# Optimization experiments

Hardware: AMD Instinct MI355X
Metric: run time of the kernel (lower is better)

The kernel has to match this reference:

```python
import jax, jax.numpy as jnp
import numpy as np

B, S, D, H = 2, 4096, 512, 8
DH = D // H  # head dim = 64

def setup_inputs() -> dict:
    key = jax.random.key(0)
    ks = jax.random.split(key, 9)
    s = 0.02
    return {
        "Q": jax.random.normal(ks[0], (B, S, D), jnp.float32),
        "Wq": jax.random.normal(ks[1], (D, D), jnp.float32) * s,
        "bq": jnp.zeros((D,), jnp.float32),
        "Wk": jax.random.normal(ks[2], (D, D), jnp.float32) * s,
        "bk": jnp.zeros((D,), jnp.float32),
        "Wv": jax.random.normal(ks[3], (D, D), jnp.float32) * s,
        "bv": jnp.zeros((D,), jnp.float32),
        "Wo": jax.random.normal(ks[4], (D, D), jnp.float32) * s,
        "bo": jnp.zeros((D,), jnp.float32),
    }

def reference(Q, Wq, bq, Wk, bk, Wv, bv, Wo, bo):
    bs, s, d = Q.shape
    scale = DH ** -0.5
    # torch Linear: x @ W.T + b, W is [out, in]
    q = (Q @ Wq.T + bq).reshape(bs, s, H, DH).transpose(0, 2, 1, 3)  # [b,h,s,dh]
    k = (Q @ Wk.T + bk).reshape(bs, s, H, DH).transpose(0, 2, 1, 3)
    v = (Q @ Wv.T + bv).reshape(bs, s, H, DH).transpose(0, 2, 1, 3)
    scores = jnp.einsum('bhqd,bhkd->bhqk', q, k) * scale  # [b,h,s,s]
    attn = jax.nn.softmax(scores, axis=-1)
    out = jnp.einsum('bhqk,bhkd->bhqd', attn, v)  # [b,h,s,dh]
    out = out.transpose(0, 2, 1, 3).reshape(bs, s, H * DH)
    out = out @ Wo.T + bo
    return (out, attn)
```

## Files before the change

### kernel.cpp

```cpp
#include <hip/hip_runtime.h>
#include <hip/hip_bf16.h>

#define B_  2
#define S_  4096
#define D_  512
#define H_  8
#define DH_ 64
#define BH_ 16
#define M_  (B_*S_)

typedef __attribute__((ext_vector_type(4))) float f32x4;
typedef __attribute__((ext_vector_type(8))) short s16x8;
typedef __attribute__((ext_vector_type(4))) short s16x4;

#define MFMA(A,Bv,C) __builtin_amdgcn_mfma_f32_16x16x32_bf16(A,Bv,C,0,0,0)

typedef const void __attribute__((address_space(1)))* gas_t;
typedef void __attribute__((address_space(3)))* las_t;
#define GLDS(gp, lp) __builtin_amdgcn_global_load_lds((gas_t)(gp), (las_t)(lp), 16, 0, 0)

static __device__ __forceinline__ unsigned short f2bf(float f){
    union { float f; unsigned int u; } v; v.f = f;
    unsigned int r = (v.u + 0x7FFFu + ((v.u >> 16) & 1u)) >> 16;
    return (unsigned short)r;
}
static __device__ __forceinline__ float bf2f(unsigned short b){
    union { unsigned int u; float f; } v; v.u = ((unsigned int)b) << 16;
    return v.f;
}

__global__ __launch_bounds__(256) void cvt_bf16(const float* __restrict__ src,
                                                unsigned short* __restrict__ dst, int n4){
    int i = blockIdx.x * 256 + threadIdx.x;
    if (i < n4){
        float4 v = reinterpret_cast<const float4*>(src)[i];
        ushort4 o;
        o.x = f2bf(v.x); o.y = f2bf(v.y); o.z = f2bf(v.z); o.w = f2bf(v.w);
        reinterpret_cast<ushort4*>(dst)[i] = o;
    }
}

__global__ __launch_bounds__(256) void gemm_bt(const unsigned short* __restrict__ A,
                                               const unsigned short* __restrict__ W,
                                               const float* __restrict__ bias,
                                               unsigned short* __restrict__ dst_bf,
                                               float* __restrict__ dst_f32){
    const int mt = blockIdx.x, nt0 = blockIdx.y;
    const int wave = threadIdx.x >> 6, lane = threadIdx.x & 63;
    const int g = lane >> 4, r16 = lane & 15;
    const unsigned short* Ap = A + (size_t)(mt*64 + wave*16 + r16) * 512;

    f32x4 acc[4];
    #pragma unroll
    for (int i = 0; i < 4; ++i) acc[i] = (f32x4){0.f,0.f,0.f,0.f};

    #pragma unroll
    for (int k0 = 0; k0 < 512; k0 += 64){
        s16x8 a0 = *(const s16x8*)(Ap + k0 + g*8);
        s16x8 a1 = *(const s16x8*)(Ap + k0 + 32 + g*8);
        #pragma unroll
        for (int nt = 0; nt < 4; ++nt){
            const unsigned short* Wp = W + (size_t)(nt0*64 + nt*16 + r16)*512 + k0 + g*8;
            s16x8 b0 = *(const s16x8*)(Wp);
            s16x8 b1 = *(const s16x8*)(Wp + 32);
            acc[nt] = MFMA(a0, b0, acc[nt]);
            acc[nt] = MFMA(a1, b1, acc[nt]);
        }
    }

    #pragma unroll
    for (int nt = 0; nt < 4; ++nt){
        const int col = nt0*64 + nt*16 + r16;
        const float bv = bias[col];
        #pragma unroll
        for (int r = 0; r < 4; ++r){
            const int orow = mt*64 + wave*16 + g*4 + r;
            float val = acc[nt][r] + bv;
            if (dst_f32){
                dst_f32[(size_t)orow*512 + col] = val;
            } else {
                const int b = orow >> 12, s = orow & 4095;
                const int h = col >> 6,  dh = col & 63;
                dst_bf[((size_t)(b*H_ + h)*S_ + s)*DH_ + dh] = f2bf(val);
            }
        }
    }
}

__global__ __launch_bounds__(256) void transpose_v(const unsigned short* __restrict__ vh,
                                                   unsigned short* __restrict__ vT){
    __shared__ unsigned short tile[64][65];
    const int bh = blockIdx.y, s0 = blockIdx.x * 64;
    const int t = threadIdx.x, c = t & 63, r4 = t >> 6;
    const unsigned short* src = vh + (size_t)bh*S_*DH_;
    #pragma unroll
    for (int i = 0; i < 16; ++i){
        int sr = i*4 + r4;
        tile[sr][c] = src[(size_t)(s0 + sr)*DH_ + c];
    }
    __syncthreads();
    unsigned short* dst = vT + (size_t)bh*DH_*S_;
    #pragma unroll
    for (int i = 0; i < 16; ++i){
        int d = i*4 + r4;
        dst[(size_t)d*S_ + s0 + c] = tile[c][d];
    }
}

__global__ __launch_bounds__(512, 4) void attn_fused(const unsigned short* __restrict__ qh,
                                                     const unsigned short* __restrict__ kh,
                                                     const unsigned short* __restrict__ vT,
                                                     float* __restrict__ attn,
                                                     unsigned short* __restrict__ ctx){
    __shared__ unsigned short Kb[2][64][64];
    __shared__ unsigned short Vb[2][64][64];
    __shared__ unsigned short Pbf[8][16][68];

    const int lin = blockIdx.y * 32 + blockIdx.x;
    const int nl  = (lin & 7) * 64 + (lin >> 3);
    const int qt  = nl & 31;
    const int bh  = nl >> 5;

    const int wave = threadIdx.x >> 6, lane = threadIdx.x & 63;
    const int g = lane >> 4, r16 = lane & 15;
    const float SCALE = 0.125f;

    const unsigned short* qbase = qh + (size_t)bh*S_*DH_;
    const unsigned short* kbase = kh + (size_t)bh*S_*DH_;
    const unsigned short* vbase = vT + (size_t)bh*DH_*S_;

    const int tr = wave*8 + (lane >> 3);
    const int cc = (lane & 7) ^ (tr & 7);
    unsigned short* kl[2] = { &Kb[0][wave*8][0], &Kb[1][wave*8][0] };
    unsigned short* vl[2] = { &Vb[0][wave*8][0], &Vb[1][wave*8][0] };

    const int sw = r16 & 7;
    const int c0 = (g ^ sw) * 8;
    const int c1 = ((4 + g) ^ sw) * 8;

    const int qrow = qt*128 + wave*16 + r16;
    s16x8 qa0 = *(const s16x8*)(qbase + (size_t)qrow*DH_ + g*8);
    s16x8 qa1 = *(const s16x8*)(qbase + (size_t)qrow*DH_ + 32 + g*8);

    GLDS(kbase + (size_t)tr*DH_ + cc*8, kl[0]);
    asm volatile("s_waitcnt vmcnt(0)" ::: "memory");
    __builtin_amdgcn_s_barrier();
    __builtin_amdgcn_sched_barrier(0);

    float lsum[4] = {0.f,0.f,0.f,0.f};
    for (int t = 0; t < 64; ++t){
        const int nxt = (t + 1) & 63;
        GLDS(kbase + (size_t)(nxt*64 + tr)*DH_ + cc*8, kl[(t&1)^1]);
        __builtin_amdgcn_sched_barrier(0);
        const unsigned short (*Kt)[64] = Kb[t&1];
        #pragma unroll
        for (int nt = 0; nt < 4; ++nt){
            const int row = nt*16 + r16;
            s16x8 b0 = *(const s16x8*)(&Kt[row][c0]);
            s16x8 b1 = *(const s16x8*)(&Kt[row][c1]);
            f32x4 acc = (f32x4){0.f,0.f,0.f,0.f};
            acc = MFMA(qa0, b0, acc);
            acc = MFMA(qa1, b1, acc);
            #pragma unroll
            for (int r = 0; r < 4; ++r) lsum[r] += __expf(acc[r]*SCALE);
        }
        asm volatile("s_waitcnt vmcnt(0)" ::: "memory");
        __builtin_amdgcn_s_barrier();
        __builtin_amdgcn_sched_barrier(0);
    }

    #pragma unroll
    for (int m = 1; m < 16; m <<= 1){
        #pragma unroll
        for (int r = 0; r < 4; ++r) lsum[r] += __shfl_xor(lsum[r], m, 64);
    }
    float inv[4];
    #pragma unroll
    for (int r = 0; r < 4; ++r) inv[r] = 1.0f / lsum[r];

    f32x4 oacc[4];
    #pragma unroll
    for (int i = 0; i < 4; ++i) oacc[i] = (f32x4){0.f,0.f,0.f,0.f};

    GLDS(vbase + (size_t)tr*S_ + cc*8, vl[0]);
    asm volatile("s_waitcnt vmcnt(0)" ::: "memory");
    __builtin_amdgcn_s_barrier();
    __builtin_amdgcn_sched_barrier(0);

    float* attnW = attn + ((size_t)bh*S_ + qt*128 + wave*16)*S_;
    unsigned short (*Pw)[68] = Pbf[wave];

    for (int t = 0; t < 64; ++t){
        const int nxt = (t + 1) & 63;
        GLDS(kbase + (size_t)(nxt*64 + tr)*DH_ + cc*8, kl[(t&1)^1]);
        GLDS(vbase + (size_t)tr*S_ + nxt*64 + cc*8,    vl[(t&1)^1]);
        __builtin_amdgcn_sched_barrier(0);
        const unsigned short (*Kt)[64] = Kb[t&1];
        const unsigned short (*Vt)[64] = Vb[t&1];

        f32x4 pacc[4];
        #pragma unroll
        for (int nt = 0; nt < 4; ++nt){
            const int row = nt*16 + r16;
            s16x8 b0 = *(const s16x8*)(&Kt[row][c0]);
            s16x8 b1 = *(const s16x8*)(&Kt[row][c1]);
            f32x4 acc = (f32x4){0.f,0.f,0.f,0.f};
            acc = MFMA(qa0, b0, acc);
            acc = MFMA(qa1, b1, acc);
            pacc[nt] = acc;
        }
        #pragma unroll
        for (int nt = 0; nt < 4; ++nt){
            #pragma unroll
            for (int r = 0; r < 4; ++r){
                float p = __expf(pacc[nt][r]*SCALE) * inv[r];
                Pw[g*4 + r][nt*16 + r16] = f2bf(p);
            }
        }
        s16x4 plo0 = *(const s16x4*)(&Pw[r16][g*8]);
        s16x4 phi0 = *(const s16x4*)(&Pw[r16][g*8 + 4]);
        s16x4 plo1 = *(const s16x4*)(&Pw[r16][32 + g*8]);
        s16x4 phi1 = *(const s16x4*)(&Pw[r16][32 + g*8 + 4]);
        s16x8 pa0 = __builtin_shufflevector(plo0, phi0, 0,1,2,3,4,5,6,7);
        s16x8 pa1 = __builtin_shufflevector(plo1, phi1, 0,1,2,3,4,5,6,7);
        #pragma unroll
        for (int i = 0; i < 4; ++i){
            const int row = i*4 + g;
            s16x4 pb = *(const s16x4*)(&Pw[row][r16*4]);
            f32x4 o;
            #pragma unroll
            for (int j = 0; j < 4; ++j) o[j] = bf2f((unsigned short)pb[j]);
            __builtin_nontemporal_store(o, (f32x4*)(attnW + (size_t)row*S_ + t*64 + r16*4));
        }
        #pragma unroll
        for (int nt = 0; nt < 4; ++nt){
            const int row = nt*16 + r16;
            s16x8 v0 = *(const s16x8*)(&Vt[row][c0]);
            s16x8 v1 = *(const s16x8*)(&Vt[row][c1]);
            oacc[nt] = MFMA(pa0, v0, oacc[nt]);
            oacc[nt] = MFMA(pa1, v1, oacc[nt]);
        }
        asm volatile("s_waitcnt vmcnt(4)" ::: "memory");
        __builtin_amdgcn_s_barrier();
        __builtin_amdgcn_sched_barrier(0);
    }

    const int b = bh >> 3, h = bh & 7;
    #pragma unroll
    for (int nt = 0; nt < 4; ++nt){
        #pragma unroll
        for (int r = 0; r < 4; ++r){
            const int qr = qt*128 + wave*16 + g*4 + r;
            ctx[(size_t)(b*S_ + qr)*D_ + h*64 + nt*16 + r16] = f2bf(oacc[nt][r]);
        }
    }
}

extern "C" void kernel_launch(void* const* d_in, const int* in_sizes, int n_in,
                              void* d_out, int out_size, void* d_ws, size_t ws_size,
                              hipStream_t stream){
    const float* Q  = (const float*)d_in[0];
    const float* Wq = (const float*)d_in[1];
    const float* bq = (const float*)d_in[2];
    const float* Wk = (const float*)d_in[3];
    const float* bk = (const float*)d_in[4];
    const float* Wv = (const float*)d_in[5];
    const float* bv = (const float*)d_in[6];
    const float* Wo = (const float*)d_in[7];
    const float* bo = (const float*)d_in[8];

    float* out  = (float*)d_out;
    float* attn = out + (size_t)M_*D_;

    unsigned short* Qbf = (unsigned short*)attn;
    unsigned short* Wqb = Qbf + (size_t)M_*D_;
    unsigned short* Wkb = Wqb + 512*512;
    unsigned short* Wvb = Wkb + 512*512;
    unsigned short* vh  = Wvb + 512*512;

    unsigned short* qhb = (unsigned short*)d_ws;
    unsigned short* khb = qhb + (size_t)BH_*S_*DH_;
    unsigned short* vTb = khb + (size_t)BH_*S_*DH_;
    unsigned short* ctx = vTb + (size_t)BH_*S_*DH_;
    unsigned short* Wob = ctx + (size_t)M_*D_;

    cvt_bf16<<<dim3(M_*D_/4/256), 256, 0, stream>>>(Q,  Qbf, M_*D_/4);
    cvt_bf16<<<dim3(512*512/4/256), 256, 0, stream>>>(Wq, Wqb, 512*512/4);
    cvt_bf16<<<dim3(512*512/4/256), 256, 0, stream>>>(Wk, Wkb, 512*512/4);
    cvt_bf16<<<dim3(512*512/4/256), 256, 0, stream>>>(Wv, Wvb, 512*512/4);
    cvt_bf16<<<dim3(512*512/4/256), 256, 0, stream>>>(Wo, Wob, 512*512/4);

    dim3 pg(M_/64, D_/64);
    gemm_bt<<<pg, 256, 0, stream>>>(Qbf, Wqb, bq, qhb, nullptr);
    gemm_bt<<<pg, 256, 0, stream>>>(Qbf, Wkb, bk, khb, nullptr);
    gemm_bt<<<pg, 256, 0, stream>>>(Qbf, Wvb, bv, vh,  nullptr);

    transpose_v<<<dim3(S_/64, BH_), 256, 0, stream>>>(vh, vTb);

    attn_fused<<<dim3(32, BH_), 512, 0, stream>>>(qhb, khb, vTb, attn, ctx);

    gemm_bt<<<pg, 256, 0, stream>>>(ctx, Wob, bo, nullptr, out);
}
```

Baseline: 421.3 us.

## Batch attention-probability stores across tile pairs, use exp2, merge weight conversions

The second attention pass now double-buffers the per-wave probability tile in LDS and writes the fp32 attention matrix every two tiles, so each row write covers 128 contiguous columns (512 bytes) and the stores overlap the next tile's compute. The P fragments for the PV MFMA are read with single 16-byte LDS loads instead of split loads. Exponentials use the hardware exp2 with the scale folded into a log2e constant, and the four weight conversions are merged into one launch. The vmcnt wait counts were adjusted to match, which risks ordering mistakes and uses more LDS.

```diff
diff --git a/kernel.cpp b/kernel.cpp
--- a/kernel.cpp
+++ b/kernel.cpp
@@ -18,6 +18,8 @@
 typedef const void __attribute__((address_space(1)))* gas_t;
 typedef void __attribute__((address_space(3)))* las_t;
 #define GLDS(gp, lp) __builtin_amdgcn_global_load_lds((gas_t)(gp), (las_t)(lp), 16, 0, 0)
+
+#define EXP_C 0.18033688011112042f
 
 static __device__ __forceinline__ unsigned short f2bf(float f){
     union { float f; unsigned int u; } v; v.f = f;
@@ -38,6 +40,24 @@
         o.x = f2bf(v.x); o.y = f2bf(v.y); o.z = f2bf(v.z); o.w = f2bf(v.w);
         reinterpret_cast<ushort4*>(dst)[i] = o;
     }
+}
+
+__global__ __launch_bounds__(256) void cvt_w4(const float* __restrict__ s0, const float* __restrict__ s1,
+                                              const float* __restrict__ s2, const float* __restrict__ s3,
+                                              unsigned short* __restrict__ d0, unsigned short* __restrict__ d1,
+                                              unsigned short* __restrict__ d2, unsigned short* __restrict__ d3){
+    const float* s; unsigned short* d;
+    switch (blockIdx.y){
+        case 0: s = s0; d = d0; break;
+        case 1: s = s1; d = d1; break;
+        case 2: s = s2; d = d2; break;
+        default: s = s3; d = d3; break;
+    }
+    int i = blockIdx.x * 256 + threadIdx.x;
+    float4 v = reinterpret_cast<const float4*>(s)[i];
+    ushort4 o;
+    o.x = f2bf(v.x); o.y = f2bf(v.y); o.z = f2bf(v.z); o.w = f2bf(v.w);
+    reinterpret_cast<ushort4*>(d)[i] = o;
 }
 
 __global__ __launch_bounds__(256) void gemm_bt(const unsigned short* __restrict__ A,
@@ -114,7 +134,7 @@
                                                      unsigned short* __restrict__ ctx){
     __shared__ unsigned short Kb[2][64][64];
     __shared__ unsigned short Vb[2][64][64];
-    __shared__ unsigned short Pbf[8][16][68];
+    __shared__ __align__(16) unsigned short Pbf[8][16][136];
 
     const int lin = blockIdx.y * 32 + blockIdx.x;
     const int nl  = (lin & 7) * 64 + (lin >> 3);
@@ -123,7 +143,6 @@
 
     const int wave = threadIdx.x >> 6, lane = threadIdx.x & 63;
     const int g = lane >> 4, r16 = lane & 15;
-    const float SCALE = 0.125f;
 
     const unsigned short* qbase = qh + (size_t)bh*S_*DH_;
     const unsigned short* kbase = kh + (size_t)bh*S_*DH_;
@@ -162,7 +181,8 @@
             acc = MFMA(qa0, b0, acc);
             acc = MFMA(qa1, b1, acc);
             #pragma unroll
-            for (int r = 0; r < 4; ++r) lsum[r] += __expf(acc[r]*SCALE);
+            for (int r = 0; r < 4; ++r)
+                lsum[r] += __builtin_amdgcn_exp2f(acc[r]*EXP_C);
         }
         asm volatile("s_waitcnt vmcnt(0)" ::: "memory");
         __builtin_amdgcn_s_barrier();
@@ -188,16 +208,13 @@
     __builtin_amdgcn_sched_barrier(0);
 
     float* attnW = attn + ((size_t)bh*S_ + qt*128 + wave*16)*S_;
-    unsigned short (*Pw)[68] = Pbf[wave];
-
-    for (int t = 0; t < 64; ++t){
-        const int nxt = (t + 1) & 63;
-        GLDS(kbase + (size_t)(nxt*64 + tr)*DH_ + cc*8, kl[(t&1)^1]);
-        GLDS(vbase + (size_t)tr*S_ + nxt*64 + cc*8,    vl[(t&1)^1]);
-        __builtin_amdgcn_sched_barrier(0);
+    unsigned short (*Pw)[136] = Pbf[wave];
+    const int sl = lane & 31, sh = lane >> 5;
+
+    auto compute_tile = [&](int t){
         const unsigned short (*Kt)[64] = Kb[t&1];
         const unsigned short (*Vt)[64] = Vb[t&1];
-
+        const int cb = (t&1)*64;
         f32x4 pacc[4];
         #pragma unroll
         for (int nt = 0; nt < 4; ++nt){
@@ -213,25 +230,12 @@
         for (int nt = 0; nt < 4; ++nt){
             #pragma unroll
             for (int r = 0; r < 4; ++r){
-                float p = __expf(pacc[nt][r]*SCALE) * inv[r];
-                Pw[g*4 + r][nt*16 + r16] = f2bf(p);
+                float p = __builtin_amdgcn_exp2f(pacc[nt][r]*EXP_C) * inv[r];
+                Pw[g*4 + r][cb + nt*16 + r16] = f2bf(p);
             }
         }
-        s16x4 plo0 = *(const s16x4*)(&Pw[r16][g*8]);
-        s16x4 phi0 = *(const s16x4*)(&Pw[r16][g*8 + 4]);
-        s16x4 plo1 = *(const s16x4*)(&Pw[r16][32 + g*8]);
-        s16x4 phi1 = *(const s16x4*)(&Pw[r16][32 + g*8 + 4]);
-        s16x8 pa0 = __builtin_shufflevector(plo0, phi0, 0,1,2,3,4,5,6,7);
-        s16x8 pa1 = __builtin_shufflevector(plo1, phi1, 0,1,2,3,4,5,6,7);
-        #pragma unroll
-        for (int i = 0; i < 4; ++i){
-            const int row = i*4 + g;
-            s16x4 pb = *(const s16x4*)(&Pw[row][r16*4]);
-            f32x4 o;
-            #pragma unroll
-            for (int j = 0; j < 4; ++j) o[j] = bf2f((unsigned short)pb[j]);
-            __builtin_nontemporal_store(o, (f32x4*)(attnW + (size_t)row*S_ + t*64 + r16*4));
-        }
+        s16x8 pa0 = *(const s16x8*)(&Pw[r16][cb + g*8]);
+        s16x8 pa1 = *(const s16x8*)(&Pw[r16][cb + 32 + g*8]);
         #pragma unroll
         for (int nt = 0; nt < 4; ++nt){
             const int row = nt*16 + r16;
@@ -240,10 +244,48 @@
             oacc[nt] = MFMA(pa0, v0, oacc[nt]);
             oacc[nt] = MFMA(pa1, v1, oacc[nt]);
         }
-        asm volatile("s_waitcnt vmcnt(4)" ::: "memory");
+    };
+
+    auto store_pair = [&](int tfirst){
+        #pragma unroll
+        for (int i = 0; i < 8; ++i){
+            const int row = i*2 + sh;
+            s16x4 pb = *(const s16x4*)(&Pw[row][sl*4]);
+            f32x4 o;
+            #pragma unroll
+            for (int j = 0; j < 4; ++j) o[j] = bf2f((unsigned short)pb[j]);
+            __builtin_nontemporal_store(o,
+                (f32x4*)(attnW + (size_t)row*S_ + tfirst*64 + sl*4));
+        }
+    };
+
+    GLDS(kbase + (size_t)(1*64 + tr)*DH_ + cc*8, kl[1]);
+    GLDS(vbase + (size_t)tr*S_ + 1*64 + cc*8,    vl[1]);
+    __builtin_amdgcn_sched_barrier(0);
+    compute_tile(0);
+    asm volatile("s_waitcnt vmcnt(0)" ::: "memory");
+    __builtin_amdgcn_s_barrier();
+    __builtin_amdgcn_sched_barrier(0);
+
+    for (int t = 1; t < 64; ++t){
+        const int nxt = (t + 1) & 63;
+        GLDS(kbase + (size_t)(nxt*64 + tr)*DH_ + cc*8, kl[(t&1)^1]);
+        GLDS(vbase + (size_t)tr*S_ + nxt*64 + cc*8,    vl[(t&1)^1]);
+        __builtin_amdgcn_sched_barrier(0);
+        if ((t & 1) == 0){
+            store_pair(t - 2);
+            __builtin_amdgcn_sched_barrier(0);
+        }
+        compute_tile(t);
+        if (t & 1){
+            asm volatile("s_waitcnt vmcnt(0)" ::: "memory");
+        } else {
+            asm volatile("s_waitcnt vmcnt(8)" ::: "memory");
+        }
         __builtin_amdgcn_s_barrier();
         __builtin_amdgcn_sched_barrier(0);
     }
+    store_pair(62);
 
     const int b = bh >> 3, h = bh & 7;
     #pragma unroll
@@ -284,11 +326,8 @@
     unsigned short* ctx = vTb + (size_t)BH_*S_*DH_;
     unsigned short* Wob = ctx + (size_t)M_*D_;
 
-    cvt_bf16<<<dim3(M_*D_/4/256), 256, 0, stream>>>(Q,  Qbf, M_*D_/4);
-    cvt_bf16<<<dim3(512*512/4/256), 256, 0, stream>>>(Wq, Wqb, 512*512/4);
-    cvt_bf16<<<dim3(512*512/4/256), 256, 0, stream>>>(Wk, Wkb, 512*512/4);
-    cvt_bf16<<<dim3(512*512/4/256), 256, 0, stream>>>(Wv, Wvb, 512*512/4);
-    cvt_bf16<<<dim3(512*512/4/256), 256, 0, stream>>>(Wo, Wob, 512*512/4);
+    cvt_bf16<<<dim3(M_*D_/4/256), 256, 0, stream>>>(Q, Qbf, M_*D_/4);
+    cvt_w4<<<dim3(512*512/4/256, 4), 256, 0, stream>>>(Wq, Wk, Wv, Wo, Wqb, Wkb, Wvb, Wob);
 
     dim3 pg(M_/64, D_/64);
     gemm_bt<<<pg, 256, 0, stream>>>(Qbf, Wqb, bq, qhb, nullptr);
```

Measured after the change: 392.1 us. -6.9%, faster.
